# Performance work log

Measured on AMD Instinct MI355X. Metric: run time of the kernel, lower is better.

## Reference

```python
import jax, jax.numpy as jnp
import numpy as np

NEG = -1e30  # log(0) surrogate that stays finite in fp32
BLANK = 0


def setup_inputs() -> dict:
    key = jax.random.key(0)
    k1, k2 = jax.random.split(key)
    B, T, V, L = 32, 1024, 1024, 256
    logits = jax.random.normal(k1, (B, T, V), dtype=jnp.float32)
    log_probs = jax.nn.log_softmax(logits, axis=-1)  # module expects log-probs
    labels = jax.random.randint(k2, (B, L), 1, V, dtype=jnp.int32)  # avoid blank=0
    input_lens = jnp.full((B,), T, dtype=jnp.int32)
    label_lens = jnp.full((B,), L, dtype=jnp.int32)
    return {"log_probs": log_probs, "labels": labels,
            "input_lens": input_lens, "label_lens": label_lens}


def _ctc_loss_sum(log_probs, labels, input_lens, label_lens, blank=BLANK):
    """CTC forward DP (alpha recursion) in log space; reduction='sum', zero_infinity=True."""
    B, T, V = log_probs.shape
    L = labels.shape[1]
    S = 2 * L + 1  # extended label: blank l1 blank l2 ... blank

    ext = jnp.full((B, S), blank, dtype=labels.dtype)
    ext = ext.at[:, 1::2].set(labels)
    # skip transition s-2 -> s allowed iff ext[s] != blank and ext[s] != ext[s-2]
    skip = jnp.concatenate(
        [jnp.zeros((B, 2), dtype=bool),
         (ext[:, 2:] != blank) & (ext[:, 2:] != ext[:, :-2])], axis=1)

    lp_tbv = jnp.transpose(log_probs, (1, 0, 2))  # 'btv->tbv' as in the module

    emit0 = jnp.take_along_axis(lp_tbv[0], ext, axis=1)  # [B,S]
    alpha0 = jnp.full((B, S), NEG, dtype=log_probs.dtype)
    alpha0 = alpha0.at[:, 0].set(emit0[:, 0]).at[:, 1].set(emit0[:, 1])

    neg1 = jnp.full((B, 1), NEG, dtype=log_probs.dtype)
    neg2 = jnp.full((B, 2), NEG, dtype=log_probs.dtype)

    def step(alpha, inputs):
        lp_t, t = inputs  # lp_t: [B,V]
        em = jnp.take_along_axis(lp_t, ext, axis=1)  # [B,S]
        a1 = alpha
        a2 = jnp.concatenate([neg1, alpha[:, :-1]], axis=1)
        a3 = jnp.where(skip, jnp.concatenate([neg2, alpha[:, :-2]], axis=1), NEG)
        new = jnp.logaddexp(jnp.logaddexp(a1, a2), a3) + em
        # freeze alpha once past this sample's input length
        new = jnp.where((t < input_lens)[:, None], new, alpha)
        return new, None

    ts = jnp.arange(1, T)
    alpha, _ = jax.lax.scan(step, alpha0, (lp_tbv[1:], ts))

    s_last = 2 * label_lens  # final blank state index per sample
    a_last = jnp.take_along_axis(alpha, s_last[:, None], axis=1)[:, 0]
    a_prev = jnp.take_along_axis(alpha, (s_last - 1)[:, None], axis=1)[:, 0]
    loss_b = -jnp.logaddexp(a_last, a_prev)
    loss_b = jnp.where(loss_b > 1e29, 0.0, loss_b)  # zero_infinity=True
    return jnp.sum(loss_b)


def reference(log_probs, labels, input_lens, label_lens):
    return _ctc_loss_sum(log_probs, labels, input_lens, label_lens)
```

## Files before the change

### kernel.cpp

```cpp
#include <hip/hip_runtime.h>


constexpr int B_ = 32, T_ = 1024, V_ = 1024, L_ = 256;
constexpr int S_ = 2 * L_ + 1;
constexpr int CH = 16;
constexpr int NCHUNK = 64;
constexpr int NBUF = 4;
constexpr float LN2F = 0.6931471805599453f;

typedef const __attribute__((address_space(1))) unsigned int* gp_t;
typedef __attribute__((address_space(3))) unsigned int* lp_t;

template <int CTRL>
__device__ __forceinline__ float dpp_fmax(float x) {
    const int t = __builtin_amdgcn_update_dpp(0, __float_as_int(x), CTRL, 0xf, 0xf, true);
    return fmaxf(x, __int_as_float(t));
}

__device__ __forceinline__ float wave_max_dpp(float x) {
    x = dpp_fmax<0x111>(x);
    x = dpp_fmax<0x112>(x);
    x = dpp_fmax<0x114>(x);
    x = dpp_fmax<0x118>(x);
    x = dpp_fmax<0x142>(x);
    x = dpp_fmax<0x143>(x);
    return __int_as_float(__builtin_amdgcn_readlane(__float_as_int(x), 63));
}

__device__ __forceinline__ float dpp_wave_shr1(float x) {
    return __int_as_float(
        __builtin_amdgcn_update_dpp(0, __float_as_int(x), 0x138, 0xf, 0xf, true));
}

__global__ __launch_bounds__(256, 4) void ctc_gather(
    float* __restrict__ lp, const int* __restrict__ labels,
    float* __restrict__ blanks)
{
    const int wave = threadIdx.x >> 6;
    const int lane = threadIdx.x & 63;
    const int r = blockIdx.x * 4 + wave;
    const int b = r >> 10;
    float* row = lp + (size_t)r * V_;
    const int* labb = labels + b * L_;

    const int4 e = *(const int4*)(labb + 4 * lane);
    const float v0 = row[e.x];
    const float v1 = row[e.y];
    const float v2 = row[e.z];
    const float v3 = row[e.w];
    const float vb = row[0];
    float4 q;
    q.x = __expf(v0); q.y = __expf(v1); q.z = __expf(v2); q.w = __expf(v3);
    const float qb = __expf(vb);
    __syncthreads();
    *(float4*)(row + 4 * lane) = q;
    if (lane == 0) {
        const int t = r & (T_ - 1);
        blanks[(r & ~(T_ - 1)) + ((t + T_ - 1) & (T_ - 1))] = qb;
    }
}

__global__ __launch_bounds__(128) void ctc_dp(
    const float* __restrict__ Q, const float* __restrict__ blanks,
    const int* __restrict__ labels, const int* __restrict__ input_lens,
    const int* __restrict__ label_lens, float* __restrict__ out)
{
    __shared__ float blk[T_ + 4];
    __shared__ float buf[NBUF][CH][256];
    __shared__ int Pf, Cf;
    const int b    = blockIdx.x;
    const int tid  = threadIdx.x;
    const int lane = tid & 63;
    const int wv   = tid >> 6;
    const float* Qb  = Q + (size_t)b * T_ * V_;
    const float* blg = blanks + b * T_;
    const int*  labb = labels + b * L_;
    const int il = input_lens[b];
    const int ll = label_lens[b];
    const int tend = il < T_ ? il : T_;

    if (tid == 0) { Pf = 0; Cf = 0; }
    __syncthreads();

    if (wv == 1) {
        #pragma unroll
        for (int i = 0; i < 4; ++i)
            __builtin_amdgcn_global_load_lds((gp_t)(blg + 256 * i + 4 * lane),
                                             (lp_t)&blk[256 * i], 16, 0, 0);
        #pragma unroll
        for (int i = 0; i < CH; ++i) {
            int t = 1 + i; if (t > T_ - 1) t = T_ - 1;
            __builtin_amdgcn_global_load_lds(
                (gp_t)(Qb + (size_t)t * V_ + 4 * lane),
                (lp_t)&buf[0][i][0], 16, 0, 0);
        }
        for (int c = 0; c < NCHUNK; ++c) {
            if (c + 1 < NCHUNK) {
                while (__hip_atomic_load(&Cf, __ATOMIC_ACQUIRE,
                                         __HIP_MEMORY_SCOPE_WORKGROUP) < c + 2 - NBUF) {}
                const int cb = (c + 1) & (NBUF - 1);
                #pragma unroll
                for (int i = 0; i < CH; ++i) {
                    int t = 1 + (c + 1) * CH + i; if (t > T_ - 1) t = T_ - 1;
                    __builtin_amdgcn_global_load_lds(
                        (gp_t)(Qb + (size_t)t * V_ + 4 * lane),
                        (lp_t)&buf[cb][i][0], 16, 0, 0);
                }
                asm volatile("s_waitcnt vmcnt(16)" ::: "memory");
            } else {
                asm volatile("s_waitcnt vmcnt(0)" ::: "memory");
            }
            if (lane == 0)
                __hip_atomic_store(&Pf, c + 1, __ATOMIC_RELEASE,
                                   __HIP_MEMORY_SCOPE_WORKGROUP);
        }
    } else {
        const int4 e  = *(const int4*)(labb + 4 * lane);
        const int  ep = (lane > 0) ? labb[4 * lane - 1] : -1;
        const float kf0 = ((8 * lane + 1) >= 3 && e.x != ep) ? 1.f : 0.f;
        const float kf1 = (e.y != e.x) ? 1.f : 0.f;
        const float kf2 = (e.z != e.y) ? 1.f : 0.f;
        const float kf3 = (e.w != e.z) ? 1.f : 0.f;
        const float bl0 = blg[T_ - 1];
        const float q00 = Qb[0];
        float p0 = (lane == 0) ? bl0 : 0.f;
        float p1 = (lane == 0) ? q00 : 0.f;
        float p2 = 0.f, p3 = 0.f, p4 = 0.f, p5 = 0.f,
              p6 = 0.f, p7 = 0.f, p8 = 0.f;
        int Esc = 0;
        float pm1 = 0.f;
        float sfP = 1.f, sfM = 1.f;

        auto snap = [&]() -> float {
            float m = fmaxf(fmaxf(fmaxf(fmaxf(p0, p1), fmaxf(p2, p3)),
                                  fmaxf(fmaxf(p4, p5), fmaxf(p6, p7))), p8);
            m = wave_max_dpp(m);
            const unsigned eb = (__float_as_uint(m) >> 23) & 0xffu;
            if (eb >= 1u && eb <= 254u) {
                unsigned k = 318u - eb;
                if (k > 254u) k = 254u;
                Esc += (int)k - 127;
                return __uint_as_float(k << 23);
            }
            return 1.f;
        };

        for (int c = 0; c < NCHUNK; ++c) {
            while (__hip_atomic_load(&Pf, __ATOMIC_ACQUIRE,
                                     __HIP_MEMORY_SCOPE_WORKGROUP) <= c) {}
            const float* base = &buf[c & (NBUF - 1)][0][0] + 4 * lane;
            float4 qA = *(const float4*)(base);
            float4 qB = *(const float4*)(base + 256);
            float4 qC = *(const float4*)(base + 512);
            float4 bv = *(const float4*)&blk[c * CH];
            float4 bvn;
            #pragma unroll
            for (int i = 0; i < CH; ++i) {
                const int g = i & 3;
                float qb = (g == 0) ? bv.x : (g == 1) ? bv.y
                         : (g == 2) ? bv.z : bv.w;
                float4 q = qA;
                qA = qB; qB = qC;
                if (i < CH - 3)
                    qC = *(const float4*)(base + (i + 3) * 256);
                if (g == 1) bvn = *(const float4*)&blk[c * CH + i + 3];
                if (g == 3) bv = bvn;
                if (i == 0) { q.x *= sfP; q.y *= sfP; q.z *= sfP; q.w *= sfP; qb *= sfP; }
                if (i == 8) { q.x *= sfM; q.y *= sfM; q.z *= sfM; q.w *= sfM; qb *= sfM; }
                const int t = 1 + c * CH + i;
                if (t < tend) {
                    const float n7 = fmaf(kf3, p5, p7 + p6) * q.w;
                    const float n8 = (p8 + p7) * qb;
                    const float pm1n = dpp_wave_shr1(n7);
                    const float n0 = (p0 + pm1) * qb;
                    const float n1 = fmaf(kf0, pm1, p1 + p0) * q.x;
                    const float n2 = (p2 + p1) * qb;
                    const float n3 = fmaf(kf1, p1, p3 + p2) * q.y;
                    const float n4 = (p4 + p3) * qb;
                    const float n5 = fmaf(kf2, p3, p5 + p4) * q.z;
                    const float n6 = (p6 + p5) * qb;
                    p0 = n0; p1 = n1; p2 = n2; p3 = n3; p4 = n4;
                    p5 = n5; p6 = n6; p7 = n7; p8 = n8; pm1 = pm1n;
                }
                if (i == 4)  sfM = snap();
                if (i == 12) sfP = snap();
            }
            if (lane == 0)
                __hip_atomic_store(&Cf, c + 1, __ATOMIC_RELEASE,
                                   __HIP_MEMORY_SCOPE_WORKGROUP);
        }
        p0 *= sfP; p1 *= sfP; p2 *= sfP; p3 *= sfP; p4 *= sfP;
        p5 *= sfP; p6 *= sfP; p7 *= sfP; p8 *= sfP;

        const int sl = 2 * ll;
        auto pick = [&](int s) -> float {
            if (s == 512) return __shfl(p8, 63);
            const int r = s & 7;
            float v = p0;
            v = (r == 1) ? p1 : v; v = (r == 2) ? p2 : v;
            v = (r == 3) ? p3 : v; v = (r == 4) ? p4 : v;
            v = (r == 5) ? p5 : v; v = (r == 6) ? p6 : v;
            v = (r == 7) ? p7 : v;
            return __shfl(v, s >> 3);
        };
        const float la = pick(sl);
        const float lb = pick(sl - 1);
        if (lane == 0) {
            const float tot = la + lb;
            float loss = (float)Esc * LN2F - __logf(tot);
            if (!(loss <= 1e29f)) loss = 0.f;
            atomicAdd(out, loss);
        }
    }
}

extern "C" void kernel_launch(void* const* d_in, const int* in_sizes, int n_in,
                              void* d_out, int out_size, void* d_ws, size_t ws_size,
                              hipStream_t stream) {
    float*       lp     = (float*)d_in[0];
    const int*   labels = (const int*)d_in[1];
    const int*   il     = (const int*)d_in[2];
    const int*   ll     = (const int*)d_in[3];
    float* out    = (float*)d_out;
    float* blanks = (float*)d_ws;

    hipMemsetAsync(out, 0, sizeof(float), stream);
    ctc_gather<<<dim3(B_ * T_ / 4), dim3(256), 0, stream>>>(lp, labels, blanks);
    ctc_dp<<<dim3(B_), dim3(128), 0, stream>>>(lp, blanks, labels, il, ll, out);
}
```

Before: 300.5 us.

## Stage gather rows through LDS and batch-prefetch whole chunk into registers

The gather kernel now loads each full log-prob row coalesced into shared memory and performs the label gather from LDS, replacing scattered global reads. It also drops the block-wide barrier before the in-place write. In the DP kernel, all 16 timestep float4 values and the blank values of a chunk are loaded into registers up front, fenced by sched barriers, instead of a rolling three-deep prefetch. This trades more register pressure and a longer up-front LDS burst for fewer latency stalls inside the serial recurrence. It also moves the sequential per-timestep work off LDS wait chains.

Measured after the change: 309.0 us. +2.8%, slower.

```diff
diff --git a/kernel.cpp b/kernel.cpp
--- a/kernel.cpp
+++ b/kernel.cpp
@@ -36,27 +36,35 @@
     float* __restrict__ lp, const int* __restrict__ labels,
     float* __restrict__ blanks)
 {
+    __shared__ float rows[4][V_];
     const int wave = threadIdx.x >> 6;
     const int lane = threadIdx.x & 63;
     const int r = blockIdx.x * 4 + wave;
     const int b = r >> 10;
     float* row = lp + (size_t)r * V_;
     const int* labb = labels + b * L_;
-
     const int4 e = *(const int4*)(labb + 4 * lane);
-    const float v0 = row[e.x];
-    const float v1 = row[e.y];
-    const float v2 = row[e.z];
-    const float v3 = row[e.w];
-    const float vb = row[0];
+
+    const float4 v0 = *(const float4*)(row + 4 * lane);
+    const float4 v1 = *(const float4*)(row + 256 + 4 * lane);
+    const float4 v2 = *(const float4*)(row + 512 + 4 * lane);
+    const float4 v3 = *(const float4*)(row + 768 + 4 * lane);
+    float* slab = &rows[wave][0];
+    *(float4*)(slab + 4 * lane)       = v0;
+    *(float4*)(slab + 256 + 4 * lane) = v1;
+    *(float4*)(slab + 512 + 4 * lane) = v2;
+    *(float4*)(slab + 768 + 4 * lane) = v3;
+    const float g0 = slab[e.x];
+    const float g1 = slab[e.y];
+    const float g2 = slab[e.z];
+    const float g3 = slab[e.w];
+    const float gb = slab[0];
     float4 q;
-    q.x = __expf(v0); q.y = __expf(v1); q.z = __expf(v2); q.w = __expf(v3);
-    const float qb = __expf(vb);
-    __syncthreads();
+    q.x = __expf(g0); q.y = __expf(g1); q.z = __expf(g2); q.w = __expf(g3);
     *(float4*)(row + 4 * lane) = q;
     if (lane == 0) {
         const int t = r & (T_ - 1);
-        blanks[(r & ~(T_ - 1)) + ((t + T_ - 1) & (T_ - 1))] = qb;
+        blanks[(r & ~(T_ - 1)) + ((t + T_ - 1) & (T_ - 1))] = __expf(gb);
     }
 }
 
@@ -149,22 +157,24 @@
             while (__hip_atomic_load(&Pf, __ATOMIC_ACQUIRE,
                                      __HIP_MEMORY_SCOPE_WORKGROUP) <= c) {}
             const float* base = &buf[c & (NBUF - 1)][0][0] + 4 * lane;
-            float4 qA = *(const float4*)(base);
-            float4 qB = *(const float4*)(base + 256);
-            float4 qC = *(const float4*)(base + 512);
-            float4 bv = *(const float4*)&blk[c * CH];
-            float4 bvn;
+
+            __builtin_amdgcn_sched_barrier(0);
+            float4 rq[CH]; float4 bl4[4];
+            #pragma unroll
+            for (int j = 0; j < CH; ++j)
+                rq[j] = *(const float4*)(base + j * 256);
+            #pragma unroll
+            for (int j = 0; j < 4; ++j)
+                bl4[j] = *(const float4*)&blk[c * CH + 4 * j];
+            __builtin_amdgcn_sched_barrier(0);
+
             #pragma unroll
             for (int i = 0; i < CH; ++i) {
                 const int g = i & 3;
+                const float4 bv = bl4[i >> 2];
                 float qb = (g == 0) ? bv.x : (g == 1) ? bv.y
                          : (g == 2) ? bv.z : bv.w;
-                float4 q = qA;
-                qA = qB; qB = qC;
-                if (i < CH - 3)
-                    qC = *(const float4*)(base + (i + 3) * 256);
-                if (g == 1) bvn = *(const float4*)&blk[c * CH + i + 3];
-                if (g == 3) bv = bvn;
+                float4 q = rq[i];
                 if (i == 0) { q.x *= sfP; q.y *= sfP; q.z *= sfP; q.w *= sfP; qb *= sfP; }
                 if (i == 8) { q.x *= sfM; q.y *= sfM; q.z *= sfM; q.w *= sfM; qb *= sfM; }
                 const int t = 1 + c * CH + i;
```
